# Kernel optimization log

Measured on AMD Instinct MI355X. Metric: run time of the kernel, lower is better.

Reference implementation:

```python
import jax, jax.numpy as jnp
import numpy as np

TOP_K = 2


def setup_inputs() -> dict:
    key = jax.random.key(0)
    ks = jax.random.split(key, 6)
    B, T, H, E, F = 2, 2048, 1024, 8, 4096
    s1 = 1.0 / np.sqrt(H)
    s2 = 1.0 / np.sqrt(F)
    return {
        "hidden_states": jax.random.normal(ks[0], (B, T, H), dtype=jnp.float32),
        "router_w": jax.random.normal(ks[1], (E, H), dtype=jnp.float32) * s1,
        "w1": jax.random.normal(ks[2], (E, H, F), dtype=jnp.float32) * s1,
        "b1": jnp.zeros((E, F), dtype=jnp.float32),
        "w2": jax.random.normal(ks[3], (E, F, H), dtype=jnp.float32) * s2,
        "b2": jnp.zeros((E, H), dtype=jnp.float32),
    }


def reference(hidden_states, router_w, w1, b1, w2, b2):
    # hidden_states: [B,T,H]; router_w: [E,H]; w1: [E,H,F]; w2: [E,F,H]
    E = router_w.shape[0]
    K = TOP_K
    dt = hidden_states.dtype

    # Router
    router_logits = jnp.einsum("bth,eh->bte", hidden_states, router_w)  # [B,T,E]
    topk_values, topk_indices = jax.lax.top_k(router_logits, K)         # [B,T,K]
    topk_weights = jax.nn.softmax(topk_values.astype(jnp.float32), axis=-1).astype(dt)

    # Dense all-expert MLP (module computes every expert on every token)
    h_mid = jax.nn.gelu(
        jnp.einsum("bth,ehf->btef", hidden_states, w1) + b1, approximate=False
    )  # [B,T,E,F]
    expert_outputs = jnp.einsum("btef,efh->bteh", h_mid, w2) + b2  # [B,T,E,H]

    # Gather top-K expert outputs and combine
    topk_out = jnp.take_along_axis(expert_outputs, topk_indices[..., None], axis=2)  # [B,T,K,H]
    mixed_output = jnp.sum(topk_out * topk_weights[..., None], axis=2)  # [B,T,H]

    # Load-balancing aux loss
    router_probs = jax.nn.softmax(router_logits.astype(jnp.float32), axis=-1)
    P = router_probs.mean(axis=(0, 1))                       # [E]
    hard = jax.nn.one_hot(topk_indices, E, dtype=jnp.float32)  # [B,T,K,E]
    f = hard.mean(axis=(0, 1, 2))                            # [E]
    aux_loss = jnp.float32(E) * jnp.sum(f * P)

    # concept_mat is None in a fresh module -> statement loss is exactly 0
    statement_loss = jnp.float32(0.0)
    return mixed_output, aux_loss, statement_loss
```

## Files before the change

kernel.cpp:

```cpp
#include <hip/hip_runtime.h>


typedef unsigned short ushort_t;
typedef __attribute__((ext_vector_type(2))) float f32x2;
typedef __attribute__((ext_vector_type(4))) unsigned int u32x4;
typedef __attribute__((ext_vector_type(4))) unsigned short u16x4;
typedef __attribute__((ext_vector_type(4))) float f32x4;
typedef __attribute__((ext_vector_type(8))) __bf16 bf16x8;

#define NTOK 4096
#define HD   1024
#define FD   4096
#define NE   8
#define NKTOT 8192

__device__ __forceinline__ ushort_t f2bf(float f) {
  unsigned u = __builtin_bit_cast(unsigned, f);
  u += 0x7fffu + ((u >> 16) & 1u);
  return (ushort_t)(u >> 16);
}
__device__ __forceinline__ unsigned pk2(float a, float b) {
  unsigned r;
  asm("v_cvt_pk_bf16_f32 %0, %1, %2" : "=v"(r) : "v"(a), "v"(b));
  return r;
}
__device__ __forceinline__ float bf2f(ushort_t u) {
  unsigned v = ((unsigned)u) << 16;
  return __builtin_bit_cast(float, v);
}
__device__ __forceinline__ bf16x8 frag_ld(const void* p) {
  u32x4 v = *reinterpret_cast<const u32x4*>(p);
  return __builtin_bit_cast(bf16x8, v);
}

#define GLOAD16(g, l) __builtin_amdgcn_global_load_lds(                         \
    (const __attribute__((address_space(1))) unsigned int*)(g),                 \
    (__attribute__((address_space(3))) unsigned int*)(l), 16, 0, 0)

#define WAITVM4()  asm volatile("s_waitcnt vmcnt(4)" ::: "memory")
#define WAITVM0()  asm volatile("s_waitcnt vmcnt(0)" ::: "memory")
#define BARRIER() do { asm volatile("s_waitcnt lgkmcnt(0)" ::: "memory");       \
                       __builtin_amdgcn_s_barrier(); } while (0)

__global__ void init_k(int* counts) {
  if (threadIdx.x < NE) counts[threadIdx.x] = 0;
}

__global__ void convx_k(const float* __restrict__ src, ushort_t* __restrict__ dst) {
  const size_t i = ((size_t)blockIdx.x * 256 + threadIdx.x) * 4;
  const f32x4 v = *reinterpret_cast<const f32x4*>(src + i);
  u16x4 o;
  o.x = f2bf(v.x); o.y = f2bf(v.y); o.z = f2bf(v.z); o.w = f2bf(v.w);
  *reinterpret_cast<u16x4*>(dst + i) = o;
}

__global__ void router_k(const float* __restrict__ x, const float* __restrict__ rw,
                         float* __restrict__ tokP, int* __restrict__ counts,
                         int* __restrict__ tk_e, int* __restrict__ tk_s,
                         float* __restrict__ tk_w) {
  const int w = threadIdx.x >> 6, l = threadIdx.x & 63;
  const int t = blockIdx.x * 4 + w;
  const float* xr = x + (size_t)t * HD;
  float acc[NE];
#pragma unroll
  for (int e = 0; e < NE; ++e) acc[e] = 0.f;
  for (int it = 0; it < HD / 64; ++it) {
    const int h = l + it * 64;
    const float xv = xr[h];
#pragma unroll
    for (int e = 0; e < NE; ++e) acc[e] = fmaf(xv, rw[e * HD + h], acc[e]);
  }
#pragma unroll
  for (int e = 0; e < NE; ++e) {
#pragma unroll
    for (int s = 32; s > 0; s >>= 1) acc[e] += __shfl_xor(acc[e], s, 64);
  }
  float m = acc[0];
#pragma unroll
  for (int e = 1; e < NE; ++e) m = fmaxf(m, acc[e]);
  float ssum = 0.f;
  float p[NE];
#pragma unroll
  for (int e = 0; e < NE; ++e) { p[e] = expf(acc[e] - m); ssum += p[e]; }
  const float inv = 1.f / ssum;
  if (l < NE) tokP[(size_t)t * NE + l] = p[l] * inv;

  if (l == 0) {
    int i0 = 0; float v0 = acc[0];
#pragma unroll
    for (int e = 1; e < NE; ++e) if (acc[e] > v0) { v0 = acc[e]; i0 = e; }
    int i1 = -1; float v1 = -3.4e38f;
#pragma unroll
    for (int e = 0; e < NE; ++e) if (e != i0 && acc[e] > v1) { v1 = acc[e]; i1 = e; }
    const float w0 = 1.f / (1.f + expf(v1 - v0));
    const int s0 = atomicAdd(&counts[i0], 1);
    const int s1 = atomicAdd(&counts[i1], 1);
    tk_e[2 * t] = i0;     tk_s[2 * t] = s0;     tk_w[2 * t] = w0;
    tk_e[2 * t + 1] = i1; tk_s[2 * t + 1] = s1; tk_w[2 * t + 1] = 1.f - w0;
  }
}

__global__ void finalize_k(const float* __restrict__ tokP, const int* __restrict__ counts,
                           int* __restrict__ offsets, float* __restrict__ out_tail) {
  __shared__ float red[16][8];
  const int tid = threadIdx.x;
  f32x4 a0 = {0.f, 0.f, 0.f, 0.f}, a1 = {0.f, 0.f, 0.f, 0.f};
#pragma unroll
  for (int k = 0; k < 4; ++k) {
    const float* p = tokP + ((size_t)tid * 4 + k) * 8;
    a0 += *reinterpret_cast<const f32x4*>(p);
    a1 += *reinterpret_cast<const f32x4*>(p + 4);
  }
#pragma unroll
  for (int s = 1; s < 64; s <<= 1) {
#pragma unroll
    for (int c = 0; c < 4; ++c) {
      a0[c] += __shfl_xor(a0[c], s, 64);
      a1[c] += __shfl_xor(a1[c], s, 64);
    }
  }
  if ((tid & 63) == 0) {
    const int wv = tid >> 6;
#pragma unroll
    for (int c = 0; c < 4; ++c) { red[wv][c] = a0[c]; red[wv][4 + c] = a1[c]; }
  }
  __syncthreads();
  if (tid == 0) {
    float P[8];
    for (int c = 0; c < 8; ++c) {
      float s = 0.f;
      for (int q = 0; q < 16; ++q) s += red[q][c];
      P[c] = s * (1.f / NTOK);
    }
    int off = 0; float aux = 0.f;
    for (int q = 0; q < NE; ++q) { offsets[q] = off; off += counts[q]; }
    for (int q = 0; q < NE; ++q) aux += ((float)counts[q] / (float)NKTOT) * P[q];
    out_tail[0] = (float)NE * aux;
    out_tail[1] = 0.f;
  }
}

__global__ void build_slots_k(const int* __restrict__ tk_e, const int* __restrict__ tk_s,
                              const int* __restrict__ offsets, int* __restrict__ slot_token) {
  const int i = blockIdx.x * 256 + threadIdx.x;
  const int e = tk_e[i];
  slot_token[offsets[e] + tk_s[i]] = i >> 1;
}

template <bool IS_G1>
__global__ __launch_bounds__(512, 4) void moe_fused(
    const ushort_t* __restrict__ A, const float* __restrict__ W,
    const float* __restrict__ bias,
    const int* __restrict__ counts, const int* __restrict__ offsets,
    const int* __restrict__ slot_token,
    ushort_t* __restrict__ midout, ushort_t* __restrict__ ybuf) {
  constexpr int KDF = IS_G1 ? HD : FD;
  constexpr int WST = IS_G1 ? FD : HD;
  constexpr int NSTEP = IS_G1 ? 16 : 32;
  const int id = blockIdx.x;
  const int e = id & 7;
  const int q = id >> 3;
  const int ty = q % 5;
  const int r = q / 5;
  const int np = IS_G1 ? r : (r >> 1);
  const int ks = IS_G1 ? 0 : (r & 1);
  const int n0 = np * 128;
  const int KB = ks * 2048;
  const int cnt = counts[e];
  if (ty * 256 >= cnt) return;
  const int off = offsets[e];
  const int pos0 = off + ty * 256;
  const int rr = cnt - ty * 256;
  const int rows_rem = rr < 256 ? rr : 256;

  __shared__ __align__(16) ushort_t lds[40960];

  const int tid = threadIdx.x;
  const int w = tid >> 6, l = tid & 63;
  const int wr = w >> 1, wc = w & 1;

  const int sw = (((l & 7) ^ ((l >> 3) & 7)) << 4);
  const char* ab[4];
#pragma unroll
  for (int c = 0; c < 4; ++c) {
    const int row = c * 64 + w * 8 + (l >> 3);
    int pos = pos0 + row; if (pos > NKTOT - 1) pos = NKTOT - 1;
    const size_t ar = IS_G1 ? (size_t)slot_token[pos] : (size_t)pos;
    ab[c] = (const char*)A + (ar * KDF + KB) * 2 + sw;
  }

  const float* wB = W + (size_t)e * ((size_t)HD * FD) +
                    ((size_t)KB + 8 * w) * WST + n0 + 2 * l;

  f32x4 acc[4][4] = {};
  f32x2 R[8];

  auto stageA = [&](int tt) {
    const int bb = tt & 1;
#pragma unroll
    for (int c = 0; c < 4; ++c)
      GLOAD16(ab[c] + tt * 128, &lds[bb * 16384 + (c * 64 + w * 8) * 64]);
  };
  auto issueB = [&](int tt) {
    const float* p = wB + (size_t)tt * 64 * WST;
#pragma unroll
    for (int i = 0; i < 8; ++i)
      R[i] = *reinterpret_cast<const f32x2*>(p + (size_t)i * WST);
  };
  auto writeB = [&]() {
    ushort_t* d = &lds[32768 + (2 * l) * 64 + ((w ^ (l & 7)) << 3)];
    u32x4 v;
    v.x = pk2(R[0].x, R[1].x); v.y = pk2(R[2].x, R[3].x);
    v.z = pk2(R[4].x, R[5].x); v.w = pk2(R[6].x, R[7].x);
    *reinterpret_cast<u32x4*>(d) = v;
    v.x = pk2(R[0].y, R[1].y); v.y = pk2(R[2].y, R[3].y);
    v.z = pk2(R[4].y, R[5].y); v.w = pk2(R[6].y, R[7].y);
    *reinterpret_cast<u32x4*>(d + 64) = v;
  };
  auto compute = [&](int tt) {
    const ushort_t* Ab = &lds[(tt & 1) * 16384];
    const ushort_t* Bb = &lds[32768];
    const int arow = wr * 64 + (l & 15);
    const int brow = wc * 64 + (l & 15);
    const int ax = l & 7;
    const int bx = (l >> 1) & 7;
    __builtin_amdgcn_s_setprio(1);
#pragma unroll
    for (int kk = 0; kk < 2; ++kk) {
      const int kc = kk * 4 + (l >> 4);
      bf16x8 afr[4];
#pragma unroll
      for (int mm = 0; mm < 4; ++mm)
        afr[mm] = frag_ld(&Ab[(arow + mm * 16) * 64 + ((kc ^ ax) << 3)]);
#pragma unroll
      for (int nn = 0; nn < 4; ++nn) {
        const bf16x8 bfr = frag_ld(&Bb[(brow + nn * 16) * 64 + ((kc ^ bx) << 3)]);
#pragma unroll
        for (int mm = 0; mm < 4; ++mm)
          acc[mm][nn] = __builtin_amdgcn_mfma_f32_16x16x32_bf16(
              afr[mm], bfr, acc[mm][nn], 0, 0, 0);
      }
    }
    __builtin_amdgcn_s_setprio(0);
  };

  issueB(0);
  stageA(0);
  WAITVM4();
  writeB();
  WAITVM0();
  BARRIER();

  for (int t = 0; t < NSTEP - 1; ++t) {
    issueB(t + 1);
    stageA(t + 1);
    __builtin_amdgcn_sched_barrier(0);
    compute(t);
    __builtin_amdgcn_s_barrier();
    WAITVM4();
    writeB();
    WAITVM0();
    BARRIER();
  }
  compute(NSTEP - 1);
  __builtin_amdgcn_s_barrier();

  {
    const int lr4 = (l >> 4) * 4, lc = l & 15;
#pragma unroll
    for (int nn = 0; nn < 4; ++nn) {
      const int col = wc * 64 + nn * 16 + lc;
      const float bv = IS_G1 ? bias[(size_t)e * FD + n0 + col] : 0.f;
#pragma unroll
      for (int mm = 0; mm < 4; ++mm) {
        const int rb = wr * 64 + mm * 16 + lr4;
#pragma unroll
        for (int j = 0; j < 4; ++j) {
          float v = acc[mm][nn][j] + bv;
          if (IS_G1) v = 0.5f * v * (1.0f + erff(v * 0.70710678118654752f));
          lds[(rb + j) * 128 + col] = f2bf(v);
        }
      }
    }
    BARRIER();
#pragma unroll
    for (int p = 0; p < 8; ++p) {
      const int idx = p * 4096 + tid * 8;
      const int row = idx >> 7;
      const int col = idx & 127;
      if (row < rows_rem) {
        const u32x4 v = *reinterpret_cast<const u32x4*>(&lds[idx]);
        if (IS_G1)
          *reinterpret_cast<u32x4*>(&midout[(size_t)(pos0 + row) * FD + n0 + col]) = v;
        else
          *reinterpret_cast<u32x4*>(
              &ybuf[((size_t)ks * NKTOT + pos0 + row) * HD + n0 + col]) = v;
      }
    }
  }
}

__global__ void combine_k(const ushort_t* __restrict__ ybuf, const int* __restrict__ tk_e,
                          const int* __restrict__ tk_s, const float* __restrict__ tk_w,
                          const int* __restrict__ offsets, const float* __restrict__ b2,
                          float* __restrict__ out) {
  const int t = blockIdx.x;
  const int e0 = tk_e[2 * t], e1 = tk_e[2 * t + 1];
  const size_t p0 = (size_t)offsets[e0] + tk_s[2 * t];
  const size_t p1 = (size_t)offsets[e1] + tk_s[2 * t + 1];
  const float w0 = tk_w[2 * t], w1v = tk_w[2 * t + 1];
  const int h = threadIdx.x * 4;
  f32x4 s0 = *reinterpret_cast<const f32x4*>(b2 + (size_t)e0 * HD + h);
  f32x4 s1 = *reinterpret_cast<const f32x4*>(b2 + (size_t)e1 * HD + h);
#pragma unroll
  for (int ks = 0; ks < 2; ++ks) {
    const u16x4 a = *reinterpret_cast<const u16x4*>(
        &ybuf[((size_t)ks * NKTOT + p0) * HD + h]);
    const u16x4 b = *reinterpret_cast<const u16x4*>(
        &ybuf[((size_t)ks * NKTOT + p1) * HD + h]);
    s0.x += bf2f(a.x); s0.y += bf2f(a.y); s0.z += bf2f(a.z); s0.w += bf2f(a.w);
    s1.x += bf2f(b.x); s1.y += bf2f(b.y); s1.z += bf2f(b.z); s1.w += bf2f(b.w);
  }
  f32x4 o = s0 * w0 + s1 * w1v;
  *reinterpret_cast<f32x4*>(out + (size_t)t * HD + h) = o;
}

extern "C" void kernel_launch(void* const* d_in, const int* in_sizes, int n_in,
                              void* d_out, int out_size, void* d_ws, size_t ws_size,
                              hipStream_t stream) {
  const float* x  = (const float*)d_in[0];
  const float* rw = (const float*)d_in[1];
  const float* w1 = (const float*)d_in[2];
  const float* b1 = (const float*)d_in[3];
  const float* w2 = (const float*)d_in[4];
  const float* b2 = (const float*)d_in[5];
  float* out = (float*)d_out;

  char* ws = (char*)d_ws;
  ushort_t* Xbf  = (ushort_t*)(ws + 0);
  ushort_t* midb = (ushort_t*)(ws + 8388608);
  ushort_t* ybuf = (ushort_t*)(ws + 75497472);
  char* sm = ws + 209715200;
  int*   counts  = (int*)(sm);
  int*   offsets = (int*)(sm + 64);
  float* tokP    = (float*)(sm + 128);
  int*   tk_e    = (int*)(sm + 128 + 131072);
  int*   tk_s    = (int*)(sm + 128 + 131072 + 32768);
  float* tk_w    = (float*)(sm + 128 + 131072 + 65536);
  int*   slot_token = (int*)(sm + 128 + 131072 + 98304);

  init_k<<<1, 64, 0, stream>>>(counts);
  convx_k<<<4096, 256, 0, stream>>>(x, Xbf);
  router_k<<<1024, 256, 0, stream>>>(x, rw, tokP, counts, tk_e, tk_s, tk_w);
  finalize_k<<<1, 1024, 0, stream>>>(tokP, counts, offsets, out + (size_t)NTOK * HD);
  build_slots_k<<<32, 256, 0, stream>>>(tk_e, tk_s, offsets, slot_token);
  moe_fused<true><<<1280, 512, 0, stream>>>(
      Xbf, w1, b1, counts, offsets, slot_token, midb, (ushort_t*)nullptr);
  moe_fused<false><<<640, 512, 0, stream>>>(
      midb, w2, b2, counts, offsets, slot_token, (ushort_t*)nullptr, ybuf);
  combine_k<<<4096, 256, 0, stream>>>(ybuf, tk_e, tk_s, tk_w, offsets, b2, out);
}
```

Before: 397.8 us.

## Shrink MoE GEMM tiles to 128x128 with 256-thread blocks and double-buffered B

```diff
diff --git a/kernel.cpp b/kernel.cpp
--- a/kernel.cpp
+++ b/kernel.cpp
@@ -2,7 +2,6 @@
 
 
 typedef unsigned short ushort_t;
-typedef __attribute__((ext_vector_type(2))) float f32x2;
 typedef __attribute__((ext_vector_type(4))) unsigned int u32x4;
 typedef __attribute__((ext_vector_type(4))) unsigned short u16x4;
 typedef __attribute__((ext_vector_type(4))) float f32x4;
@@ -37,7 +36,7 @@
     (const __attribute__((address_space(1))) unsigned int*)(g),                 \
     (__attribute__((address_space(3))) unsigned int*)(l), 16, 0, 0)
 
-#define WAITVM4()  asm volatile("s_waitcnt vmcnt(4)" ::: "memory")
+#define WAITVM2()  asm volatile("s_waitcnt vmcnt(2)" ::: "memory")
 #define WAITVM0()  asm volatile("s_waitcnt vmcnt(0)" ::: "memory")
 #define BARRIER() do { asm volatile("s_waitcnt lgkmcnt(0)" ::: "memory");       \
                        __builtin_amdgcn_s_barrier(); } while (0)
@@ -148,7 +147,7 @@
 }
 
 template <bool IS_G1>
-__global__ __launch_bounds__(512, 4) void moe_fused(
+__global__ __launch_bounds__(256, 4) void moe_fused(
     const ushort_t* __restrict__ A, const float* __restrict__ W,
     const float* __restrict__ bias,
     const int* __restrict__ counts, const int* __restrict__ offsets,
@@ -156,98 +155,94 @@
     ushort_t* __restrict__ midout, ushort_t* __restrict__ ybuf) {
   constexpr int KDF = IS_G1 ? HD : FD;
   constexpr int WST = IS_G1 ? FD : HD;
-  constexpr int NSTEP = IS_G1 ? 16 : 32;
+  constexpr int NSTEP = IS_G1 ? 32 : 64;
   const int id = blockIdx.x;
   const int e = id & 7;
   const int q = id >> 3;
-  const int ty = q % 5;
-  const int r = q / 5;
+  const int ty = q % 10;
+  const int r = q / 10;
   const int np = IS_G1 ? r : (r >> 1);
   const int ks = IS_G1 ? 0 : (r & 1);
   const int n0 = np * 128;
   const int KB = ks * 2048;
   const int cnt = counts[e];
-  if (ty * 256 >= cnt) return;
+  if (ty * 128 >= cnt) return;
   const int off = offsets[e];
-  const int pos0 = off + ty * 256;
-  const int rr = cnt - ty * 256;
-  const int rows_rem = rr < 256 ? rr : 256;
-
-  __shared__ __align__(16) ushort_t lds[40960];
+  const int pos0 = off + ty * 128;
+  const int rr = cnt - ty * 128;
+  const int rows_rem = rr < 128 ? rr : 128;
+
+  __shared__ __align__(16) ushort_t lds[16384];
 
   const int tid = threadIdx.x;
   const int w = tid >> 6, l = tid & 63;
   const int wr = w >> 1, wc = w & 1;
 
-  const int sw = (((l & 7) ^ ((l >> 3) & 7)) << 4);
-  const char* ab[4];
-#pragma unroll
-  for (int c = 0; c < 4; ++c) {
-    const int row = c * 64 + w * 8 + (l >> 3);
+  const int sw = (((l & 3) ^ ((l >> 3) & 3)) << 4);
+  const char* ab[2];
+#pragma unroll
+  for (int c = 0; c < 2; ++c) {
+    const int row = c * 64 + w * 16 + (l >> 2);
     int pos = pos0 + row; if (pos > NKTOT - 1) pos = NKTOT - 1;
     const size_t ar = IS_G1 ? (size_t)slot_token[pos] : (size_t)pos;
     ab[c] = (const char*)A + (ar * KDF + KB) * 2 + sw;
   }
 
-  const float* wB = W + (size_t)e * ((size_t)HD * FD) +
-                    ((size_t)KB + 8 * w) * WST + n0 + 2 * l;
+  const float* wBl = W + (size_t)e * ((size_t)HD * FD) +
+                     ((size_t)KB + 8 * w) * WST + n0 + l;
 
   f32x4 acc[4][4] = {};
-  f32x2 R[8];
+  float R[16];
 
   auto stageA = [&](int tt) {
-    const int bb = tt & 1;
-#pragma unroll
-    for (int c = 0; c < 4; ++c)
-      GLOAD16(ab[c] + tt * 128, &lds[bb * 16384 + (c * 64 + w * 8) * 64]);
+    ushort_t* base = &lds[(tt & 1) * 4096];
+    GLOAD16(ab[0] + tt * 64, base + (w * 16) * 32);
+    GLOAD16(ab[1] + tt * 64, base + (64 + w * 16) * 32);
   };
   auto issueB = [&](int tt) {
-    const float* p = wB + (size_t)tt * 64 * WST;
-#pragma unroll
-    for (int i = 0; i < 8; ++i)
-      R[i] = *reinterpret_cast<const f32x2*>(p + (size_t)i * WST);
+    const float* p = wBl + (size_t)tt * 32 * WST;
+#pragma unroll
+    for (int i = 0; i < 8; ++i) {
+      R[i]     = p[(size_t)i * WST];
+      R[8 + i] = p[(size_t)i * WST + 64];
+    }
   };
-  auto writeB = [&]() {
-    ushort_t* d = &lds[32768 + (2 * l) * 64 + ((w ^ (l & 7)) << 3)];
+  auto writeB = [&](int tt) {
+    ushort_t* base = &lds[8192 + (tt & 1) * 4096];
     u32x4 v;
-    v.x = pk2(R[0].x, R[1].x); v.y = pk2(R[2].x, R[3].x);
-    v.z = pk2(R[4].x, R[5].x); v.w = pk2(R[6].x, R[7].x);
-    *reinterpret_cast<u32x4*>(d) = v;
-    v.x = pk2(R[0].y, R[1].y); v.y = pk2(R[2].y, R[3].y);
-    v.z = pk2(R[4].y, R[5].y); v.w = pk2(R[6].y, R[7].y);
-    *reinterpret_cast<u32x4*>(d + 64) = v;
+    v.x = pk2(R[0], R[1]); v.y = pk2(R[2], R[3]);
+    v.z = pk2(R[4], R[5]); v.w = pk2(R[6], R[7]);
+    *reinterpret_cast<u32x4*>(base + w * 1024 + l * 8) = v;
+    v.x = pk2(R[8], R[9]);   v.y = pk2(R[10], R[11]);
+    v.z = pk2(R[12], R[13]); v.w = pk2(R[14], R[15]);
+    *reinterpret_cast<u32x4*>(base + w * 1024 + (64 + l) * 8) = v;
   };
   auto compute = [&](int tt) {
-    const ushort_t* Ab = &lds[(tt & 1) * 16384];
-    const ushort_t* Bb = &lds[32768];
+    const ushort_t* Ab = &lds[(tt & 1) * 4096];
+    const ushort_t* Bb = &lds[8192 + (tt & 1) * 4096];
     const int arow = wr * 64 + (l & 15);
-    const int brow = wc * 64 + (l & 15);
-    const int ax = l & 7;
-    const int bx = (l >> 1) & 7;
+    const int kcA = (l >> 4) ^ ((l >> 1) & 3);
+    const int bidx = (l >> 4) * 1024 + (wc * 64 + (l & 15)) * 8;
+    bf16x8 afr[4];
+#pragma unroll
+    for (int mm = 0; mm < 4; ++mm)
+      afr[mm] = frag_ld(&Ab[(arow + mm * 16) * 32 + (kcA << 3)]);
     __builtin_amdgcn_s_setprio(1);
 #pragma unroll
-    for (int kk = 0; kk < 2; ++kk) {
-      const int kc = kk * 4 + (l >> 4);
-      bf16x8 afr[4];
+    for (int nn = 0; nn < 4; ++nn) {
+      const bf16x8 bfr = frag_ld(&Bb[bidx + nn * 128]);
 #pragma unroll
       for (int mm = 0; mm < 4; ++mm)
-        afr[mm] = frag_ld(&Ab[(arow + mm * 16) * 64 + ((kc ^ ax) << 3)]);
-#pragma unroll
-      for (int nn = 0; nn < 4; ++nn) {
-        const bf16x8 bfr = frag_ld(&Bb[(brow + nn * 16) * 64 + ((kc ^ bx) << 3)]);
-#pragma unroll
-        for (int mm = 0; mm < 4; ++mm)
-          acc[mm][nn] = __builtin_amdgcn_mfma_f32_16x16x32_bf16(
-              afr[mm], bfr, acc[mm][nn], 0, 0, 0);
-      }
+        acc[mm][nn] = __builtin_amdgcn_mfma_f32_16x16x32_bf16(
+            afr[mm], bfr, acc[mm][nn], 0, 0, 0);
     }
     __builtin_amdgcn_s_setprio(0);
   };
 
   issueB(0);
   stageA(0);
-  WAITVM4();
-  writeB();
+  WAITVM2();
+  writeB(0);
   WAITVM0();
   BARRIER();
 
@@ -256,9 +251,8 @@
     stageA(t + 1);
     __builtin_amdgcn_sched_barrier(0);
     compute(t);
-    __builtin_amdgcn_s_barrier();
-    WAITVM4();
-    writeB();
+    WAITVM2();
+    writeB(t + 1);
     WAITVM0();
     BARRIER();
   }
@@ -285,7 +279,7 @@
     BARRIER();
 #pragma unroll
     for (int p = 0; p < 8; ++p) {
-      const int idx = p * 4096 + tid * 8;
+      const int idx = p * 2048 + tid * 8;
       const int row = idx >> 7;
       const int col = idx & 127;
       if (row < rows_rem) {
@@ -354,9 +348,9 @@
   router_k<<<1024, 256, 0, stream>>>(x, rw, tokP, counts, tk_e, tk_s, tk_w);
   finalize_k<<<1, 1024, 0, stream>>>(tokP, counts, offsets, out + (size_t)NTOK * HD);
   build_slots_k<<<32, 256, 0, stream>>>(tk_e, tk_s, offsets, slot_token);
-  moe_fused<true><<<1280, 512, 0, stream>>>(
+  moe_fused<true><<<2560, 256, 0, stream>>>(
       Xbf, w1, b1, counts, offsets, slot_token, midb, (ushort_t*)nullptr);
-  moe_fused<false><<<640, 512, 0, stream>>>(
+  moe_fused<false><<<1280, 256, 0, stream>>>(
       midb, w2, b2, counts, offsets, slot_token, (ushort_t*)nullptr, ybuf);
   combine_k<<<4096, 256, 0, stream>>>(ybuf, tk_e, tk_s, tk_w, offsets, b2, out);
 }
```

New measurement: 422.3 us. +6.2%, slower.
